# Performance work log

Measured on AMD Instinct MI355X. Metric: run time of the kernel, lower is better.

The kernel has to match this reference:

```python
import jax, jax.numpy as jnp
import numpy as np

VOCAB, EMB, ENC = 100000, 256, 256
N_INTENTS, N_SLOTS, LEN_INTENT = 64, 128, 64
B, S = 64, 128


def setup_inputs() -> dict:
    key = jax.random.key(0)
    ks = jax.random.split(key, 8)
    sc = 0.02
    return {
        "token_ids": jax.random.randint(ks[0], (B, S), 0, VOCAB),
        "all_intents": jax.random.randint(ks[1], (B,), 0, N_INTENTS),
        "emb_table": jax.random.normal(ks[2], (VOCAB, EMB), jnp.float32) * sc,
        "doc_enc_W": jax.random.normal(ks[3], (EMB, ENC), jnp.float32) * sc,
        "doc_enc_b": jnp.zeros((ENC,), jnp.float32),
        "slot_enc_W": jax.random.normal(ks[4], (EMB, ENC), jnp.float32) * sc,
        "slot_enc_b": jnp.zeros((ENC,), jnp.float32),
        "doc_dec_W": jax.random.normal(ks[5], (ENC, N_INTENTS), jnp.float32) * sc,
        "doc_dec_b": jnp.zeros((N_INTENTS,), jnp.float32),
        "slot_dec_W": jax.random.normal(ks[6], (ENC + LEN_INTENT, N_SLOTS), jnp.float32) * sc,
        "slot_dec_b": jnp.zeros((N_SLOTS,), jnp.float32),
    }


def reference(token_ids, all_intents, emb_table, doc_enc_W, doc_enc_b,
              slot_enc_W, slot_enc_b, doc_dec_W, doc_dec_b,
              slot_dec_W, slot_dec_b):
    # word embedding lookup: [B, S, EMB] (memory-bound gather)
    emb = emb_table[token_ids]
    # doc encoder: pool sentence then project (batched stand-in for the
    # per-sentence python loop in the original encode())
    sent = jnp.mean(emb, axis=1)                                    # [B, EMB]
    sent_enc = jax.nn.relu(sent @ doc_enc_W + doc_enc_b)            # [B, ENC]
    # intent logits (doc_decoder applied per sentence)
    intent_batch = sent_enc @ doc_dec_W + doc_dec_b                 # [B, N_INTENTS]
    # slot encoder: per-word projection (batched stand-in for per-word loop)
    word_enc = jax.nn.relu(jnp.einsum('bse,eh->bsh', emb, slot_enc_W) + slot_enc_b)
    # use_intent: one-hot of given intent appended to every word encoding
    add_feats = jax.nn.one_hot(all_intents, LEN_INTENT, dtype=word_enc.dtype)  # [B, LEN_INTENT]
    add_feats = jnp.broadcast_to(add_feats[:, None, :], (B, S, LEN_INTENT))
    slot_in = jnp.concatenate([word_enc, add_feats], axis=-1)       # [B, S, ENC+LEN_INTENT]
    slots = jnp.einsum('bsh,ho->bso', slot_in, slot_dec_W) + slot_dec_b
    slots_batch = slots.reshape(B * S, N_SLOTS)  # torch.cat along dim 0 over words
    return intent_batch, slots_batch
```

## Files before the change

kernel.cpp:

```cpp
#include <hip/hip_runtime.h>
#include <hip/hip_bf16.h>

typedef __attribute__((ext_vector_type(8))) short bf16x8;
typedef __attribute__((ext_vector_type(4))) float f32x4;

#define BATCH 64
#define SEQ   128
#define EMB   256
#define ENC   256
#define NIN   64
#define NSL   128

#define W1P_OFF   0
#define W2P_OFF   65536
#define DW1P_OFF  98304
#define DW2P_OFF  163840

#define PACK(W, NCOLS, DST, IDX) {                                            \
    const int n  = (IDX) & ((NCOLS) - 1);                                     \
    const int bk = (IDX) / (NCOLS);                                           \
    union { bf16x8 v; __hip_bfloat16 h[8]; } u;                               \
    _Pragma("unroll")                                                         \
    for (int j = 0; j < 8; ++j)                                               \
        u.h[j] = __float2bfloat16((W)[(bk * 8 + j) * (NCOLS) + n]);           \
    *(bf16x8*)((DST) + (size_t)(IDX) * 8) = u.v; }

__global__ __launch_bounds__(256) void prep_kernel(
    const float* __restrict__ slot_enc_W,
    const float* __restrict__ slot_dec_W,
    const float* __restrict__ doc_enc_W,
    const float* __restrict__ doc_dec_W,
    __hip_bfloat16* __restrict__ ws)
{
    const int tid = blockIdx.x * 256 + threadIdx.x;
    if (tid < 8192) {
        PACK(slot_enc_W, 256, ws + W1P_OFF,  tid);
    } else if (tid < 12288) {
        PACK(slot_dec_W, 128, ws + W2P_OFF,  tid - 8192);
    } else if (tid < 20480) {
        PACK(doc_enc_W,  256, ws + DW1P_OFF, tid - 12288);
    } else {
        PACK(doc_dec_W,   64, ws + DW2P_OFF, tid - 20480);
    }
}

static __device__ __forceinline__ bf16x8 cvt8(const float4 lo, const float4 hi) {
    union { bf16x8 v; __hip_bfloat16 h[8]; } u;
    u.h[0] = __float2bfloat16(lo.x); u.h[1] = __float2bfloat16(lo.y);
    u.h[2] = __float2bfloat16(lo.z); u.h[3] = __float2bfloat16(lo.w);
    u.h[4] = __float2bfloat16(hi.x); u.h[5] = __float2bfloat16(hi.y);
    u.h[6] = __float2bfloat16(hi.z); u.h[7] = __float2bfloat16(hi.w);
    return u.v;
}

__global__ __launch_bounds__(256) void fused_kernel(
    const int*   __restrict__ token_ids,
    const int*   __restrict__ all_intents,
    const float* __restrict__ emb_table,
    const float* __restrict__ doc_enc_b,
    const float* __restrict__ slot_enc_b,
    const float* __restrict__ doc_dec_b,
    const float* __restrict__ slot_dec_W,
    const float* __restrict__ slot_dec_b,
    const __hip_bfloat16* __restrict__ ws,
    float* __restrict__ out_intent,
    float* __restrict__ out_slots)
{
    __shared__ __align__(16) char smem[2 * 16 * 264 * 2];

    const int blk  = blockIdx.x;
    const int wave = threadIdx.x >> 6;
    const int lane = threadIdx.x & 63;
    const int l16  = lane & 15;
    const int quad = lane >> 4;

    const __hip_bfloat16* w1p  = ws + W1P_OFF;
    const __hip_bfloat16* w2p  = ws + W2P_OFF;
    const __hip_bfloat16* dw1p = ws + DW1P_OFF;
    const __hip_bfloat16* dw2p = ws + DW2P_OFF;

    if ((blk & 7) == 0) {
        float* red  = (float*)smem;
        float* sent = (float*)(smem + 4096);
        float* senc = (float*)(smem + 5120);

        const int b  = blk >> 3;
        const int t  = threadIdx.x;
        const int* toks = token_ids + b * SEQ;

        float4 accv = make_float4(0.f, 0.f, 0.f, 0.f);
        #pragma unroll 8
        for (int i = 0; i < 32; ++i) {
            const long tok = toks[wave * 32 + i];
            const float4 v = *(const float4*)(emb_table + tok * EMB + lane * 4);
            accv.x += v.x; accv.y += v.y; accv.z += v.z; accv.w += v.w;
        }
        *(float4*)(&red[wave * 256 + lane * 4]) = accv;
        __syncthreads();

        sent[t] = (red[t] + red[256 + t] + red[512 + t] + red[768 + t])
                  * (1.0f / 128.0f);
        __syncthreads();

        f32x4 dacc[4];
        #pragma unroll
        for (int nt = 0; nt < 4; ++nt) dacc[nt] = (f32x4){0.f, 0.f, 0.f, 0.f};

        #pragma unroll
        for (int ks = 0; ks < 8; ++ks) {
            const float* sp = sent + ks * 32 + quad * 8;
            const bf16x8 a = cvt8(*(const float4*)sp, *(const float4*)(sp + 4));
            const int kblk = ks * 4 + quad;
            #pragma unroll
            for (int nt = 0; nt < 4; ++nt) {
                const int n = wave * 64 + nt * 16 + l16;
                const bf16x8 bf = *(const bf16x8*)(dw1p + ((size_t)kblk * 256 + n) * 8);
                dacc[nt] = __builtin_amdgcn_mfma_f32_16x16x32_bf16(a, bf, dacc[nt], 0, 0, 0);
            }
        }
        if (quad == 0) {
            #pragma unroll
            for (int nt = 0; nt < 4; ++nt) {
                const int col = wave * 64 + nt * 16 + l16;
                senc[col] = fmaxf(dacc[nt][0] + doc_enc_b[col], 0.f);
            }
        }
        __syncthreads();

        f32x4 iacc = (f32x4){0.f, 0.f, 0.f, 0.f};
        #pragma unroll
        for (int ks = 0; ks < 8; ++ks) {
            const float* sp = senc + ks * 32 + quad * 8;
            const bf16x8 a = cvt8(*(const float4*)sp, *(const float4*)(sp + 4));
            const int kblk = ks * 4 + quad;
            const int n = wave * 16 + l16;
            const bf16x8 bf = *(const bf16x8*)(dw2p + ((size_t)kblk * 64 + n) * 8);
            iacc = __builtin_amdgcn_mfma_f32_16x16x32_bf16(a, bf, iacc, 0, 0, 0);
        }
        if (quad == 0)
            out_intent[b * NIN + wave * 16 + l16] = iacc[0] + doc_dec_b[wave * 16 + l16];
        __syncthreads();
    }

    __hip_bfloat16* lds_emb = (__hip_bfloat16*)smem;
    __hip_bfloat16* lds_we  = (__hip_bfloat16*)(smem + 16 * 264 * 2);

    const int row0 = blk * 16;

    #pragma unroll
    for (int i = 0; i < 4; ++i) {
        const int idx = i * 256 + threadIdx.x;
        const int r   = idx >> 6;
        const int c4  = idx & 63;
        const long tok = token_ids[row0 + r];
        const float4 v = *(const float4*)(emb_table + tok * EMB + c4 * 4);
        union { ushort4 s; __hip_bfloat16 h[4]; } u;
        u.h[0] = __float2bfloat16(v.x); u.h[1] = __float2bfloat16(v.y);
        u.h[2] = __float2bfloat16(v.z); u.h[3] = __float2bfloat16(v.w);
        *(ushort4*)(lds_emb + r * 264 + c4 * 4) = u.s;
    }
    __syncthreads();

    f32x4 acc[4];
    #pragma unroll
    for (int nt = 0; nt < 4; ++nt) acc[nt] = (f32x4){0.f, 0.f, 0.f, 0.f};

    const int nbase1 = wave * 64;
    #pragma unroll
    for (int ks = 0; ks < 8; ++ks) {
        const bf16x8 a0 = *(const bf16x8*)(lds_emb + l16 * 264 + ks * 32 + quad * 8);
        const int kblk = ks * 4 + quad;
        #pragma unroll
        for (int nt = 0; nt < 4; ++nt) {
            const int n = nbase1 + nt * 16 + l16;
            const bf16x8 bf = *(const bf16x8*)(w1p + ((size_t)kblk * 256 + n) * 8);
            acc[nt] = __builtin_amdgcn_mfma_f32_16x16x32_bf16(a0, bf, acc[nt], 0, 0, 0);
        }
    }

    #pragma unroll
    for (int nt = 0; nt < 4; ++nt) {
        const int col = nbase1 + nt * 16 + l16;
        const float bias = slot_enc_b[col];
        #pragma unroll
        for (int r = 0; r < 4; ++r) {
            const int row = quad * 4 + r;
            lds_we[row * 264 + col] =
                __float2bfloat16(fmaxf(acc[nt][r] + bias, 0.f));
        }
    }
    __syncthreads();

    f32x4 acc2[2];
    #pragma unroll
    for (int nt = 0; nt < 2; ++nt) acc2[nt] = (f32x4){0.f, 0.f, 0.f, 0.f};

    const int nbase2 = wave * 32;
    #pragma unroll
    for (int ks = 0; ks < 8; ++ks) {
        const bf16x8 a0 = *(const bf16x8*)(lds_we + l16 * 264 + ks * 32 + quad * 8);
        const int kblk = ks * 4 + quad;
        #pragma unroll
        for (int nt = 0; nt < 2; ++nt) {
            const int n = nbase2 + nt * 16 + l16;
            const bf16x8 bf = *(const bf16x8*)(w2p + ((size_t)kblk * 128 + n) * 8);
            acc2[nt] = __builtin_amdgcn_mfma_f32_16x16x32_bf16(a0, bf, acc2[nt], 0, 0, 0);
        }
    }

    const int intent = all_intents[blk >> 3];
    const float* hotrow = slot_dec_W + (long)(256 + intent) * NSL;

    #pragma unroll
    for (int nt = 0; nt < 2; ++nt) {
        const int col = nbase2 + nt * 16 + l16;
        const float add = slot_dec_b[col] + hotrow[col];
        #pragma unroll
        for (int r = 0; r < 4; ++r) {
            const int row = quad * 4 + r;
            out_slots[(long)(row0 + row) * NSL + col] = acc2[nt][r] + add;
        }
    }
}

extern "C" void kernel_launch(void* const* d_in, const int* in_sizes, int n_in,
                              void* d_out, int out_size, void* d_ws, size_t ws_size,
                              hipStream_t stream) {
    const int*   token_ids   = (const int*)d_in[0];
    const int*   all_intents = (const int*)d_in[1];
    const float* emb_table   = (const float*)d_in[2];
    const float* doc_enc_W   = (const float*)d_in[3];
    const float* doc_enc_b   = (const float*)d_in[4];
    const float* slot_enc_W  = (const float*)d_in[5];
    const float* slot_enc_b  = (const float*)d_in[6];
    const float* doc_dec_W   = (const float*)d_in[7];
    const float* doc_dec_b   = (const float*)d_in[8];
    const float* slot_dec_W  = (const float*)d_in[9];
    const float* slot_dec_b  = (const float*)d_in[10];

    __hip_bfloat16* ws = (__hip_bfloat16*)d_ws;
    float* out = (float*)d_out;

    prep_kernel<<<88, 256, 0, stream>>>(slot_enc_W, slot_dec_W,
                                        doc_enc_W, doc_dec_W, ws);

    fused_kernel<<<512, 256, 0, stream>>>(
        token_ids, all_intents, emb_table, doc_enc_b,
        slot_enc_b, doc_dec_b, slot_dec_W, slot_dec_b,
        ws, out, out + BATCH * NIN);
}
```

Baseline: 164.0 us.

## Merge weight packing into fused kernel via cooperative grid sync

Removes the separate prep kernel. Each block now packs 44 weight items and gathers its embedding tile, and the doc blocks also compute their pooled sentence, before a grid-wide sync. After the sync, all blocks read the packed bf16 weights. This saves one kernel launch and lets the pack overlap with the embedding gather. The block index is remapped so the doc blocks spread across the grid. The cost is a cooperative launch with a grid barrier, which requires all 512 blocks to be co-resident and adds barrier latency.

```diff
diff --git a/kernel.cpp b/kernel.cpp
--- a/kernel.cpp
+++ b/kernel.cpp
@@ -1,5 +1,8 @@
 #include <hip/hip_runtime.h>
 #include <hip/hip_bf16.h>
+#include <hip/hip_cooperative_groups.h>
+
+namespace cg = cooperative_groups;
 
 typedef __attribute__((ext_vector_type(8))) short bf16x8;
 typedef __attribute__((ext_vector_type(4))) float f32x4;
@@ -15,33 +18,26 @@
 #define W2P_OFF   65536
 #define DW1P_OFF  98304
 #define DW2P_OFF  163840
-
-#define PACK(W, NCOLS, DST, IDX) {                                            \
-    const int n  = (IDX) & ((NCOLS) - 1);                                     \
-    const int bk = (IDX) / (NCOLS);                                           \
-    union { bf16x8 v; __hip_bfloat16 h[8]; } u;                               \
-    _Pragma("unroll")                                                         \
-    for (int j = 0; j < 8; ++j)                                               \
-        u.h[j] = __float2bfloat16((W)[(bk * 8 + j) * (NCOLS) + n]);           \
-    *(bf16x8*)((DST) + (size_t)(IDX) * 8) = u.v; }
-
-__global__ __launch_bounds__(256) void prep_kernel(
-    const float* __restrict__ slot_enc_W,
-    const float* __restrict__ slot_dec_W,
-    const float* __restrict__ doc_enc_W,
-    const float* __restrict__ doc_dec_W,
+#define NPACK     22528
+
+static __device__ __forceinline__ void pack_item(
+    int item,
+    const float* __restrict__ slot_enc_W, const float* __restrict__ slot_dec_W,
+    const float* __restrict__ doc_enc_W,  const float* __restrict__ doc_dec_W,
     __hip_bfloat16* __restrict__ ws)
 {
-    const int tid = blockIdx.x * 256 + threadIdx.x;
-    if (tid < 8192) {
-        PACK(slot_enc_W, 256, ws + W1P_OFF,  tid);
-    } else if (tid < 12288) {
-        PACK(slot_dec_W, 128, ws + W2P_OFF,  tid - 8192);
-    } else if (tid < 20480) {
-        PACK(doc_enc_W,  256, ws + DW1P_OFF, tid - 12288);
-    } else {
-        PACK(doc_dec_W,   64, ws + DW2P_OFF, tid - 20480);
-    }
+    const float* W; int ncols; __hip_bfloat16* dst; int idx;
+    if (item < 8192)       { W = slot_enc_W; ncols = 256; dst = ws + W1P_OFF;  idx = item; }
+    else if (item < 12288) { W = slot_dec_W; ncols = 128; dst = ws + W2P_OFF;  idx = item - 8192; }
+    else if (item < 20480) { W = doc_enc_W;  ncols = 256; dst = ws + DW1P_OFF; idx = item - 12288; }
+    else                   { W = doc_dec_W;  ncols = 64;  dst = ws + DW2P_OFF; idx = item - 20480; }
+    const int n  = idx % ncols;
+    const int bk = idx / ncols;
+    union { bf16x8 v; __hip_bfloat16 h[8]; } u;
+    #pragma unroll
+    for (int j = 0; j < 8; ++j)
+        u.h[j] = __float2bfloat16(W[(bk * 8 + j) * ncols + n]);
+    *(bf16x8*)(dst + (size_t)idx * 8) = u.v;
 }
 
 static __device__ __forceinline__ bf16x8 cvt8(const float4 lo, const float4 hi) {
@@ -57,95 +53,39 @@
     const int*   __restrict__ token_ids,
     const int*   __restrict__ all_intents,
     const float* __restrict__ emb_table,
+    const float* __restrict__ doc_enc_W,
     const float* __restrict__ doc_enc_b,
+    const float* __restrict__ slot_enc_W,
     const float* __restrict__ slot_enc_b,
+    const float* __restrict__ doc_dec_W,
     const float* __restrict__ doc_dec_b,
     const float* __restrict__ slot_dec_W,
     const float* __restrict__ slot_dec_b,
-    const __hip_bfloat16* __restrict__ ws,
+    __hip_bfloat16* __restrict__ ws,
     float* __restrict__ out_intent,
     float* __restrict__ out_slots)
 {
     __shared__ __align__(16) char smem[2 * 16 * 264 * 2];
 
-    const int blk  = blockIdx.x;
+    const int bid  = blockIdx.x;
+    const int blk  = ((bid & 7) << 6) | (bid >> 3);
     const int wave = threadIdx.x >> 6;
     const int lane = threadIdx.x & 63;
     const int l16  = lane & 15;
     const int quad = lane >> 4;
 
-    const __hip_bfloat16* w1p  = ws + W1P_OFF;
-    const __hip_bfloat16* w2p  = ws + W2P_OFF;
-    const __hip_bfloat16* dw1p = ws + DW1P_OFF;
-    const __hip_bfloat16* dw2p = ws + DW2P_OFF;
-
-    if ((blk & 7) == 0) {
-        float* red  = (float*)smem;
-        float* sent = (float*)(smem + 4096);
-        float* senc = (float*)(smem + 5120);
-
-        const int b  = blk >> 3;
-        const int t  = threadIdx.x;
-        const int* toks = token_ids + b * SEQ;
-
-        float4 accv = make_float4(0.f, 0.f, 0.f, 0.f);
-        #pragma unroll 8
-        for (int i = 0; i < 32; ++i) {
-            const long tok = toks[wave * 32 + i];
-            const float4 v = *(const float4*)(emb_table + tok * EMB + lane * 4);
-            accv.x += v.x; accv.y += v.y; accv.z += v.z; accv.w += v.w;
-        }
-        *(float4*)(&red[wave * 256 + lane * 4]) = accv;
-        __syncthreads();
-
-        sent[t] = (red[t] + red[256 + t] + red[512 + t] + red[768 + t])
-                  * (1.0f / 128.0f);
-        __syncthreads();
-
-        f32x4 dacc[4];
-        #pragma unroll
-        for (int nt = 0; nt < 4; ++nt) dacc[nt] = (f32x4){0.f, 0.f, 0.f, 0.f};
-
-        #pragma unroll
-        for (int ks = 0; ks < 8; ++ks) {
-            const float* sp = sent + ks * 32 + quad * 8;
-            const bf16x8 a = cvt8(*(const float4*)sp, *(const float4*)(sp + 4));
-            const int kblk = ks * 4 + quad;
-            #pragma unroll
-            for (int nt = 0; nt < 4; ++nt) {
-                const int n = wave * 64 + nt * 16 + l16;
-                const bf16x8 bf = *(const bf16x8*)(dw1p + ((size_t)kblk * 256 + n) * 8);
-                dacc[nt] = __builtin_amdgcn_mfma_f32_16x16x32_bf16(a, bf, dacc[nt], 0, 0, 0);
-            }
-        }
-        if (quad == 0) {
-            #pragma unroll
-            for (int nt = 0; nt < 4; ++nt) {
-                const int col = wave * 64 + nt * 16 + l16;
-                senc[col] = fmaxf(dacc[nt][0] + doc_enc_b[col], 0.f);
-            }
-        }
-        __syncthreads();
-
-        f32x4 iacc = (f32x4){0.f, 0.f, 0.f, 0.f};
-        #pragma unroll
-        for (int ks = 0; ks < 8; ++ks) {
-            const float* sp = senc + ks * 32 + quad * 8;
-            const bf16x8 a = cvt8(*(const float4*)sp, *(const float4*)(sp + 4));
-            const int kblk = ks * 4 + quad;
-            const int n = wave * 16 + l16;
-            const bf16x8 bf = *(const bf16x8*)(dw2p + ((size_t)kblk * 64 + n) * 8);
-            iacc = __builtin_amdgcn_mfma_f32_16x16x32_bf16(a, bf, iacc, 0, 0, 0);
-        }
-        if (quad == 0)
-            out_intent[b * NIN + wave * 16 + l16] = iacc[0] + doc_dec_b[wave * 16 + l16];
-        __syncthreads();
-    }
-
     __hip_bfloat16* lds_emb = (__hip_bfloat16*)smem;
-    __hip_bfloat16* lds_we  = (__hip_bfloat16*)(smem + 16 * 264 * 2);
-
-    const int row0 = blk * 16;
+    __hip_bfloat16* lds_we  = (__hip_bfloat16*)(smem + 8448);
+    float* doc_red  = (float*)(smem + 8448);
+    float* doc_sent = (float*)(smem + 8448 + 4096);
+    float* doc_senc = (float*)(smem + 8448 + 5120);
+
+    const bool docb = (blk & 7) == 0;
+    const int  row0 = blk * 16;
+
+    if (threadIdx.x < 44)
+        pack_item(bid * 44 + threadIdx.x,
+                  slot_enc_W, slot_dec_W, doc_enc_W, doc_dec_W, ws);
 
     #pragma unroll
     for (int i = 0; i < 4; ++i) {
@@ -159,7 +99,74 @@
         u.h[2] = __float2bfloat16(v.z); u.h[3] = __float2bfloat16(v.w);
         *(ushort4*)(lds_emb + r * 264 + c4 * 4) = u.s;
     }
-    __syncthreads();
+
+    if (docb) {
+        const int b  = blk >> 3;
+        const int* toks = token_ids + b * SEQ;
+        float4 accv = make_float4(0.f, 0.f, 0.f, 0.f);
+        #pragma unroll 8
+        for (int i = 0; i < 32; ++i) {
+            const long tok = toks[wave * 32 + i];
+            const float4 v = *(const float4*)(emb_table + tok * EMB + lane * 4);
+            accv.x += v.x; accv.y += v.y; accv.z += v.z; accv.w += v.w;
+        }
+        *(float4*)(&doc_red[wave * 256 + lane * 4]) = accv;
+        __syncthreads();
+        doc_sent[threadIdx.x] =
+            (doc_red[threadIdx.x] + doc_red[256 + threadIdx.x] +
+             doc_red[512 + threadIdx.x] + doc_red[768 + threadIdx.x]) * (1.0f / 128.0f);
+    }
+
+    if (threadIdx.x < 44) __threadfence();
+    cg::this_grid().sync();
+
+    const __hip_bfloat16* w1p  = ws + W1P_OFF;
+    const __hip_bfloat16* w2p  = ws + W2P_OFF;
+    const __hip_bfloat16* dw1p = ws + DW1P_OFF;
+    const __hip_bfloat16* dw2p = ws + DW2P_OFF;
+
+    if (docb) {
+        const int b = blk >> 3;
+
+        f32x4 dacc[4];
+        #pragma unroll
+        for (int nt = 0; nt < 4; ++nt) dacc[nt] = (f32x4){0.f, 0.f, 0.f, 0.f};
+
+        #pragma unroll
+        for (int ks = 0; ks < 8; ++ks) {
+            const float* sp = doc_sent + ks * 32 + quad * 8;
+            const bf16x8 a = cvt8(*(const float4*)sp, *(const float4*)(sp + 4));
+            const int kblk = ks * 4 + quad;
+            #pragma unroll
+            for (int nt = 0; nt < 4; ++nt) {
+                const int n = wave * 64 + nt * 16 + l16;
+                const bf16x8 bf = *(const bf16x8*)(dw1p + ((size_t)kblk * 256 + n) * 8);
+                dacc[nt] = __builtin_amdgcn_mfma_f32_16x16x32_bf16(a, bf, dacc[nt], 0, 0, 0);
+            }
+        }
+        if (quad == 0) {
+            #pragma unroll
+            for (int nt = 0; nt < 4; ++nt) {
+                const int col = wave * 64 + nt * 16 + l16;
+                doc_senc[col] = fmaxf(dacc[nt][0] + doc_enc_b[col], 0.f);
+            }
+        }
+        __syncthreads();
+
+        f32x4 iacc = (f32x4){0.f, 0.f, 0.f, 0.f};
+        #pragma unroll
+        for (int ks = 0; ks < 8; ++ks) {
+            const float* sp = doc_senc + ks * 32 + quad * 8;
+            const bf16x8 a = cvt8(*(const float4*)sp, *(const float4*)(sp + 4));
+            const int kblk = ks * 4 + quad;
+            const int n = wave * 16 + l16;
+            const bf16x8 bf = *(const bf16x8*)(dw2p + ((size_t)kblk * 64 + n) * 8);
+            iacc = __builtin_amdgcn_mfma_f32_16x16x32_bf16(a, bf, iacc, 0, 0, 0);
+        }
+        if (quad == 0)
+            out_intent[b * NIN + wave * 16 + l16] = iacc[0] + doc_dec_b[wave * 16 + l16];
+        __syncthreads();
+    }
 
     f32x4 acc[4];
     #pragma unroll
@@ -239,13 +246,18 @@
     const float* slot_dec_b  = (const float*)d_in[10];
 
     __hip_bfloat16* ws = (__hip_bfloat16*)d_ws;
-    float* out = (float*)d_out;
-
-    prep_kernel<<<88, 256, 0, stream>>>(slot_enc_W, slot_dec_W,
-                                        doc_enc_W, doc_dec_W, ws);
-
-    fused_kernel<<<512, 256, 0, stream>>>(
-        token_ids, all_intents, emb_table, doc_enc_b,
-        slot_enc_b, doc_dec_b, slot_dec_W, slot_dec_b,
-        ws, out, out + BATCH * NIN);
-}
+    float* out        = (float*)d_out;
+    float* out_intent = out;
+    float* out_slots  = out + BATCH * NIN;
+
+    void* args[] = {
+        (void*)&token_ids, (void*)&all_intents, (void*)&emb_table,
+        (void*)&doc_enc_W, (void*)&doc_enc_b,
+        (void*)&slot_enc_W, (void*)&slot_enc_b,
+        (void*)&doc_dec_W, (void*)&doc_dec_b,
+        (void*)&slot_dec_W, (void*)&slot_dec_b,
+        (void*)&ws, (void*)&out_intent, (void*)&out_slots,
+    };
+    hipLaunchCooperativeKernel((const void*)fused_kernel,
+                               dim3(512), dim3(256), args, 0, stream);
+}
```

After: 251.6 us. +53.5%, slower.

## Reuse per-block embedding loads for sentence pooling via atomic last-block reduction

Applied to the files above, without the earlier changes.

Before, the first block of each batch re-gathered all 128 embedding rows to compute the mean, on top of its own tile. Now every block writes partial column sums of its 16-row tile to workspace. An atomic counter (zeroed by an extra prep block) picks the last of the 8 blocks per batch, which sums the partials and runs the doc encoder and decoder. This removes the redundant gather and evens out block load, at the cost of global atomics, fences and workspace traffic.

```diff
diff --git a/kernel.cpp b/kernel.cpp
--- a/kernel.cpp
+++ b/kernel.cpp
@@ -15,6 +15,9 @@
 #define W2P_OFF   65536
 #define DW1P_OFF  98304
 #define DW2P_OFF  163840
+#define NPACK     22528
+#define CNT_OFF_B    393216
+#define SENTP_OFF_B  524288
 
 #define PACK(W, NCOLS, DST, IDX) {                                            \
     const int n  = (IDX) & ((NCOLS) - 1);                                     \
@@ -30,8 +33,13 @@
     const float* __restrict__ slot_dec_W,
     const float* __restrict__ doc_enc_W,
     const float* __restrict__ doc_dec_W,
-    __hip_bfloat16* __restrict__ ws)
+    __hip_bfloat16* __restrict__ ws,
+    int* __restrict__ cnt)
 {
+    if (blockIdx.x == 88) {
+        if (threadIdx.x < BATCH) cnt[threadIdx.x] = 0;
+        return;
+    }
     const int tid = blockIdx.x * 256 + threadIdx.x;
     if (tid < 8192) {
         PACK(slot_enc_W, 256, ws + W1P_OFF,  tid);
@@ -63,52 +71,80 @@
     const float* __restrict__ slot_dec_W,
     const float* __restrict__ slot_dec_b,
     const __hip_bfloat16* __restrict__ ws,
+    float* __restrict__ sent_part,
+    int*   __restrict__ cnt,
     float* __restrict__ out_intent,
     float* __restrict__ out_slots)
 {
     __shared__ __align__(16) char smem[2 * 16 * 264 * 2];
+    __shared__ int lds_flag;
 
     const int blk  = blockIdx.x;
     const int wave = threadIdx.x >> 6;
     const int lane = threadIdx.x & 63;
     const int l16  = lane & 15;
     const int quad = lane >> 4;
+    const int t    = threadIdx.x;
+
+    __hip_bfloat16* lds_emb = (__hip_bfloat16*)smem;
+    __hip_bfloat16* lds_we  = (__hip_bfloat16*)(smem + 8448);
+    float* red      = (float*)(smem + 8448);
+    float* doc_sent = (float*)(smem + 8448 + 4096);
+    float* doc_senc = (float*)(smem + 8448 + 5120);
+
+    const int row0 = blk * 16;
+    const int b    = blk >> 3;
+    const int sub  = blk & 7;
 
     const __hip_bfloat16* w1p  = ws + W1P_OFF;
     const __hip_bfloat16* w2p  = ws + W2P_OFF;
     const __hip_bfloat16* dw1p = ws + DW1P_OFF;
     const __hip_bfloat16* dw2p = ws + DW2P_OFF;
 
-    if ((blk & 7) == 0) {
-        float* red  = (float*)smem;
-        float* sent = (float*)(smem + 4096);
-        float* senc = (float*)(smem + 5120);
-
-        const int b  = blk >> 3;
-        const int t  = threadIdx.x;
-        const int* toks = token_ids + b * SEQ;
-
-        float4 accv = make_float4(0.f, 0.f, 0.f, 0.f);
-        #pragma unroll 8
-        for (int i = 0; i < 32; ++i) {
-            const long tok = toks[wave * 32 + i];
-            const float4 v = *(const float4*)(emb_table + tok * EMB + lane * 4);
-            accv.x += v.x; accv.y += v.y; accv.z += v.z; accv.w += v.w;
-        }
-        *(float4*)(&red[wave * 256 + lane * 4]) = accv;
+    float4 accv = make_float4(0.f, 0.f, 0.f, 0.f);
+    #pragma unroll
+    for (int i = 0; i < 4; ++i) {
+        const int idx = i * 256 + t;
+        const int r   = idx >> 6;
+        const int c4  = idx & 63;
+        const long tok = token_ids[row0 + r];
+        const float4 v = *(const float4*)(emb_table + tok * EMB + c4 * 4);
+        accv.x += v.x; accv.y += v.y; accv.z += v.z; accv.w += v.w;
+        union { ushort4 s; __hip_bfloat16 h[4]; } u;
+        u.h[0] = __float2bfloat16(v.x); u.h[1] = __float2bfloat16(v.y);
+        u.h[2] = __float2bfloat16(v.z); u.h[3] = __float2bfloat16(v.w);
+        *(ushort4*)(lds_emb + r * 264 + c4 * 4) = u.s;
+    }
+    *(float4*)(&red[wave * 256 + (t & 63) * 4]) = accv;
+    __syncthreads();
+
+    const float colsum = red[t] + red[256 + t] + red[512 + t] + red[768 + t];
+    __hip_atomic_store(&sent_part[(b * 8 + sub) * 256 + t], colsum,
+                       __ATOMIC_RELAXED, __HIP_MEMORY_SCOPE_AGENT);
+    __threadfence();
+    __syncthreads();
+    if (t == 0) {
+        const int old = __hip_atomic_fetch_add(&cnt[b], 1,
+                            __ATOMIC_ACQ_REL, __HIP_MEMORY_SCOPE_AGENT);
+        lds_flag = (old == 7);
+    }
+    __syncthreads();
+
+    if (lds_flag) {
+        float s = 0.f;
+        #pragma unroll
+        for (int i = 0; i < 8; ++i)
+            s += __hip_atomic_load(&sent_part[(b * 8 + i) * 256 + t],
+                                   __ATOMIC_RELAXED, __HIP_MEMORY_SCOPE_AGENT);
+        doc_sent[t] = s * (1.0f / 128.0f);
         __syncthreads();
 
-        sent[t] = (red[t] + red[256 + t] + red[512 + t] + red[768 + t])
-                  * (1.0f / 128.0f);
-        __syncthreads();
-
         f32x4 dacc[4];
         #pragma unroll
         for (int nt = 0; nt < 4; ++nt) dacc[nt] = (f32x4){0.f, 0.f, 0.f, 0.f};
-
         #pragma unroll
         for (int ks = 0; ks < 8; ++ks) {
-            const float* sp = sent + ks * 32 + quad * 8;
+            const float* sp = doc_sent + ks * 32 + quad * 8;
             const bf16x8 a = cvt8(*(const float4*)sp, *(const float4*)(sp + 4));
             const int kblk = ks * 4 + quad;
             #pragma unroll
@@ -122,7 +158,7 @@
             #pragma unroll
             for (int nt = 0; nt < 4; ++nt) {
                 const int col = wave * 64 + nt * 16 + l16;
-                senc[col] = fmaxf(dacc[nt][0] + doc_enc_b[col], 0.f);
+                doc_senc[col] = fmaxf(dacc[nt][0] + doc_enc_b[col], 0.f);
             }
         }
         __syncthreads();
@@ -130,7 +166,7 @@
         f32x4 iacc = (f32x4){0.f, 0.f, 0.f, 0.f};
         #pragma unroll
         for (int ks = 0; ks < 8; ++ks) {
-            const float* sp = senc + ks * 32 + quad * 8;
+            const float* sp = doc_senc + ks * 32 + quad * 8;
             const bf16x8 a = cvt8(*(const float4*)sp, *(const float4*)(sp + 4));
             const int kblk = ks * 4 + quad;
             const int n = wave * 16 + l16;
@@ -142,25 +178,6 @@
         __syncthreads();
     }
 
-    __hip_bfloat16* lds_emb = (__hip_bfloat16*)smem;
-    __hip_bfloat16* lds_we  = (__hip_bfloat16*)(smem + 16 * 264 * 2);
-
-    const int row0 = blk * 16;
-
-    #pragma unroll
-    for (int i = 0; i < 4; ++i) {
-        const int idx = i * 256 + threadIdx.x;
-        const int r   = idx >> 6;
-        const int c4  = idx & 63;
-        const long tok = token_ids[row0 + r];
-        const float4 v = *(const float4*)(emb_table + tok * EMB + c4 * 4);
-        union { ushort4 s; __hip_bfloat16 h[4]; } u;
-        u.h[0] = __float2bfloat16(v.x); u.h[1] = __float2bfloat16(v.y);
-        u.h[2] = __float2bfloat16(v.z); u.h[3] = __float2bfloat16(v.w);
-        *(ushort4*)(lds_emb + r * 264 + c4 * 4) = u.s;
-    }
-    __syncthreads();
-
     f32x4 acc[4];
     #pragma unroll
     for (int nt = 0; nt < 4; ++nt) acc[nt] = (f32x4){0.f, 0.f, 0.f, 0.f};
@@ -208,7 +225,7 @@
         }
     }
 
-    const int intent = all_intents[blk >> 3];
+    const int intent = all_intents[b];
     const float* hotrow = slot_dec_W + (long)(256 + intent) * NSL;
 
     #pragma unroll
@@ -238,14 +255,19 @@
     const float* slot_dec_W  = (const float*)d_in[9];
     const float* slot_dec_b  = (const float*)d_in[10];
 
-    __hip_bfloat16* ws = (__hip_bfloat16*)d_ws;
+    char* wsb = (char*)d_ws;
+    __hip_bfloat16* ws        = (__hip_bfloat16*)wsb;
+    int*            cnt       = (int*)(wsb + CNT_OFF_B);
+    float*          sent_part = (float*)(wsb + SENTP_OFF_B);
+
     float* out = (float*)d_out;
 
-    prep_kernel<<<88, 256, 0, stream>>>(slot_enc_W, slot_dec_W,
-                                        doc_enc_W, doc_dec_W, ws);
+    prep_kernel<<<89, 256, 0, stream>>>(slot_enc_W, slot_dec_W,
+                                        doc_enc_W, doc_dec_W, ws, cnt);
 
     fused_kernel<<<512, 256, 0, stream>>>(
         token_ids, all_intents, emb_table, doc_enc_b,
         slot_enc_b, doc_dec_b, slot_dec_W, slot_dec_b,
-        ws, out, out + BATCH * NIN);
-}
+        ws, sent_part, cnt,
+        out, out + BATCH * NIN);
+}
```

New measurement: 195.8 us. 19.4% more time.
